# Kernel optimization log

Measured on AMD Instinct MI355X. Metric: run time of the kernel, lower is better.

The kernel has to match this reference:

```python
import jax, jax.numpy as jnp
import numpy as np

N, E, D, L, G, T = 50000, 600000, 128, 4, 512, 10
EPS = 1e-5


def setup_inputs() -> dict:
    key = jax.random.key(0)
    ks = jax.random.split(key, 20)
    s = lambda k, shp, fan: jax.random.normal(k, shp, jnp.float32) * (1.0 / np.sqrt(fan))
    inp = {
        'x': jax.random.normal(ks[0], (N, 3), jnp.float32),
        'edge_index': jax.random.randint(ks[1], (2, E), 0, N, jnp.int32),
        'batch': jnp.sort(jax.random.randint(ks[2], (N,), 0, G, jnp.int32)),
        'emb_W': s(ks[3], (3, D), 3),
        'emb_b': jnp.zeros((D,), jnp.float32),
        'conv_W': s(ks[4], (L, 12 * D, D), 12 * D),
        'conv_b': jnp.zeros((L, D), jnp.float32),
        'bn_gamma': jnp.ones((L, D), jnp.float32),
        'bn_beta': jnp.zeros((L, D), jnp.float32),
        'W1': s(ks[5], (D, D // 2), D), 'b1': jnp.zeros((D // 2,), jnp.float32),
        'W2': s(ks[6], (D // 2, D // 4), D // 2), 'b2': jnp.zeros((D // 4,), jnp.float32),
        'W3': s(ks[7], (D // 4, T), D // 4), 'b3': jnp.zeros((T,), jnp.float32),
    }
    return inp


def reference(x, edge_index, batch, emb_W, emb_b, conv_W, conv_b, bn_gamma, bn_beta,
              W1, b1, W2, b2, W3, b3):
    n = x.shape[0]
    src, dst = edge_index[0], edge_index[1]  # messages flow src(j) -> dst(i)
    deg = jax.ops.segment_sum(jnp.ones((src.shape[0],), x.dtype), dst, num_segments=n)
    delta = jnp.mean(jnp.log1p(deg))          # avg log-degree (PNA's avg_deg['log'])
    d = jnp.maximum(deg, 1.0)[:, None]        # clamp(min=1)
    log_d = jnp.log1p(d)
    amp, att = log_d / delta, delta / log_d   # amplification / attenuation scalers
    has_edge = (deg > 0)[:, None]

    h = x @ emb_W + emb_b                     # node_emb Linear(3, D)
    for l in range(conv_W.shape[0]):
        msg = h[src]                          # [E, D] gather
        s1 = jax.ops.segment_sum(msg, dst, num_segments=n)
        s2 = jax.ops.segment_sum(msg * msg, dst, num_segments=n)
        mean = s1 / d
        std = jnp.sqrt(jax.nn.relu(s2 / d - mean * mean) + EPS)
        mn = jnp.where(has_edge, jax.ops.segment_min(msg, dst, num_segments=n), 0.0)
        mx = jnp.where(has_edge, jax.ops.segment_max(msg, dst, num_segments=n), 0.0)
        aggs = jnp.concatenate([mean, mn, mx, std], axis=-1)                 # [N, 4D]
        out = jnp.concatenate([aggs, aggs * amp, aggs * att], axis=-1)       # [N, 12D]
        out = out @ conv_W[l] + conv_b[l]      # post_nn Linear(12D, D)
        mu = out.mean(axis=0)
        var = out.var(axis=0)
        out = (out - mu) * jax.lax.rsqrt(var + EPS) * bn_gamma[l] + bn_beta[l]
        h = jax.nn.relu(out) + h               # residual (dropout off: eval)

    # global_mean_pool over graphs
    gsum = jax.ops.segment_sum(h, batch, num_segments=G)
    cnt = jnp.maximum(jax.ops.segment_sum(jnp.ones((n,), h.dtype), batch, num_segments=G), 1.0)
    g = gsum / cnt[:, None]
    g = jax.nn.relu(g @ W1 + b1)
    g = jax.nn.relu(g @ W2 + b2)
    return g @ W3 + b3                         # source='image': no clamp
```

## Files before the change

### kernel.cpp

```cpp
#include <hip/hip_runtime.h>
#include <math.h>

#define NN 50000
#define NE 600000
#define DD 128
#define NL 4
#define NG 512
#define NT 10
#define EPSF 1e-5f

typedef __bf16 bf16x8 __attribute__((ext_vector_type(8)));
typedef float f32x4 __attribute__((ext_vector_type(4)));

__device__ __forceinline__ unsigned short f2bf(float x) {
    union { float f; unsigned u; } v; v.f = x;
    unsigned r = v.u + 0x7FFFu + ((v.u >> 16) & 1u);
    return (unsigned short)(r >> 16);
}
__device__ __forceinline__ unsigned pack_bf2(float a, float b) {
    return (unsigned)f2bf(a) | ((unsigned)f2bf(b) << 16);
}
__device__ __forceinline__ float bf_lo(unsigned v) {
    union { unsigned u; float f; } w; w.u = (v & 0xFFFFu) << 16; return w.f;
}
__device__ __forceinline__ float bf_hi(unsigned v) {
    union { unsigned u; float f; } w; w.u = v & 0xFFFF0000u; return w.f;
}
__device__ __forceinline__ void ld16(const void* g, void* l) {
    __builtin_amdgcn_global_load_lds(
        (const __attribute__((address_space(1))) unsigned int*)g,
        (__attribute__((address_space(3))) unsigned int*)l, 16, 0, 0);
}

__global__ void k_count(const int* __restrict__ dst, int* __restrict__ deg,
                        float* __restrict__ dsum, int E) {
    int e = blockIdx.x * blockDim.x + threadIdx.x;
    if (e == 0) *dsum = 0.f;
    if (e < E) atomicAdd(&deg[dst[e]], 1);
}

__global__ void k_scan_part(const int* __restrict__ deg, int* __restrict__ part, int n) {
    __shared__ int sm[256];
    int b = blockIdx.x, t = threadIdx.x;
    int base = b * 1024 + t * 4;
    int s = 0;
    #pragma unroll
    for (int j = 0; j < 4; j++) if (base + j < n) s += deg[base + j];
    sm[t] = s;
    __syncthreads();
    for (int off = 128; off > 0; off >>= 1) {
        if (t < off) sm[t] += sm[t + off];
        __syncthreads();
    }
    if (t == 0) part[b] = sm[0];
}

__global__ void k_scan_top(const int* __restrict__ part, int* __restrict__ offs,
                           int* __restrict__ row_ptr, int nb, int n) {
    if (threadIdx.x == 0) {
        int acc = 0;
        for (int i = 0; i < nb; i++) { offs[i] = acc; acc += part[i]; }
        row_ptr[n] = acc;
    }
}

__global__ void k_scan_apply(const int* __restrict__ deg, const int* __restrict__ offs,
                             int* __restrict__ row_ptr, int* __restrict__ cursor, int n) {
    __shared__ int sm[256];
    int b = blockIdx.x, t = threadIdx.x;
    int base = b * 1024 + t * 4;
    int v[4]; int s = 0;
    #pragma unroll
    for (int j = 0; j < 4; j++) { v[j] = (base + j < n) ? deg[base + j] : 0; s += v[j]; }
    sm[t] = s;
    __syncthreads();
    for (int off = 1; off < 256; off <<= 1) {
        int y = (t >= off) ? sm[t - off] : 0;
        __syncthreads();
        sm[t] += y;
        __syncthreads();
    }
    int run = offs[b] + sm[t] - s;
    #pragma unroll
    for (int j = 0; j < 4; j++) {
        if (base + j < n) { row_ptr[base + j] = run; cursor[base + j] = run; run += v[j]; }
    }
}

__global__ void k_fill(const int* __restrict__ src, const int* __restrict__ dst,
                       int* __restrict__ cursor, int* __restrict__ csr_src, int E) {
    int e = blockIdx.x * blockDim.x + threadIdx.x;
    if (e < E) {
        int d = dst[e];
        int pos = atomicAdd(&cursor[d], 1);
        csr_src[pos] = src[e];
    }
}

__global__ void k_delta(const int* __restrict__ deg, float* __restrict__ dsum, int n) {
    int i = blockIdx.x * blockDim.x + threadIdx.x;
    float v = (i < n) ? log1pf((float)deg[i]) : 0.f;
    #pragma unroll
    for (int off = 32; off > 0; off >>= 1) v += __shfl_down(v, off);
    if ((threadIdx.x & 63) == 0) atomicAdd(dsum, v);
}

__global__ void k_scalars(const int* __restrict__ deg, const float* __restrict__ dsum,
                          float* __restrict__ inv_d, float* __restrict__ amp,
                          float* __restrict__ att, int n) {
    int i = blockIdx.x * blockDim.x + threadIdx.x;
    if (i >= n) return;
    float delta = *dsum / (float)n;
    float d = fmaxf((float)deg[i], 1.f);
    float ld = log1pf(d);
    inv_d[i] = 1.f / d;
    amp[i] = ld / delta;
    att[i] = delta / ld;
}

__global__ void k_emb(const float* __restrict__ x, const float* __restrict__ W,
                      const float* __restrict__ b, float* __restrict__ h,
                      unsigned* __restrict__ hb2, int total2) {
    int i = blockIdx.x * blockDim.x + threadIdx.x;
    if (i >= total2) return;
    int node = i >> 6, c = (i & 63) * 2;
    float x0 = x[node * 3 + 0], x1 = x[node * 3 + 1], x2 = x[node * 3 + 2];
    float v0 = x0 * W[c] + x1 * W[DD + c] + x2 * W[2 * DD + c] + b[c];
    float v1 = x0 * W[c + 1] + x1 * W[DD + c + 1] + x2 * W[2 * DD + c + 1] + b[c + 1];
    ((float2*)h)[i] = make_float2(v0, v1);
    hb2[i] = pack_bf2(v0, v1);
}

__global__ void k_wconv(const float* __restrict__ W, unsigned short* __restrict__ Bt, int total) {
    int o = blockIdx.x * blockDim.x + threadIdx.x;
    if (o >= total) return;
    int l = o / 196608;
    int r = o % 196608;
    int j = r >> 16;
    int r2 = r & 65535;
    int n = r2 >> 9;
    int k = r2 & 511;
    Bt[o] = f2bf(W[(size_t)l * 196608 + (size_t)(j * 512 + k) * 128 + n]);
}

__global__ void k_agg(const unsigned* __restrict__ hb2, const int* __restrict__ row_ptr,
                      const int* __restrict__ csr_src, const float* __restrict__ inv_d,
                      unsigned* __restrict__ aggs_u, float* __restrict__ bn_zero) {
    int tid = threadIdx.x;
    if (blockIdx.x == 0) bn_zero[tid] = 0.f;
    int node = blockIdx.x * 4 + (tid >> 6);
    int t = tid & 63;
    int beg = row_ptr[node], end = row_ptr[node + 1];
    float s1a = 0.f, s1b = 0.f, s2a = 0.f, s2b = 0.f;
    float mna = INFINITY, mnb = INFINITY, mxa = -INFINITY, mxb = -INFINITY;
    int e = beg;
    for (; e + 1 < end; e += 2) {
        int sa = csr_src[e], sb = csr_src[e + 1];
        unsigned va = hb2[(size_t)sa * 64 + t];
        unsigned vb = hb2[(size_t)sb * 64 + t];
        float a0 = bf_lo(va), b0 = bf_hi(va);
        float a1 = bf_lo(vb), b1 = bf_hi(vb);
        s1a += a0 + a1; s2a += a0 * a0 + a1 * a1;
        mna = fminf(mna, fminf(a0, a1)); mxa = fmaxf(mxa, fmaxf(a0, a1));
        s1b += b0 + b1; s2b += b0 * b0 + b1 * b1;
        mnb = fminf(mnb, fminf(b0, b1)); mxb = fmaxf(mxb, fmaxf(b0, b1));
    }
    if (e < end) {
        int sa = csr_src[e];
        unsigned va = hb2[(size_t)sa * 64 + t];
        float a0 = bf_lo(va), b0 = bf_hi(va);
        s1a += a0; s2a += a0 * a0; mna = fminf(mna, a0); mxa = fmaxf(mxa, a0);
        s1b += b0; s2b += b0 * b0; mnb = fminf(mnb, b0); mxb = fmaxf(mxb, b0);
    }
    float id = inv_d[node];
    float meana = s1a * id, meanb = s1b * id;
    float sda = sqrtf(fmaxf(s2a * id - meana * meana, 0.f) + EPSF);
    float sdb = sqrtf(fmaxf(s2b * id - meanb * meanb, 0.f) + EPSF);
    if (beg == end) { mna = 0.f; mxa = 0.f; mnb = 0.f; mxb = 0.f; }
    unsigned* outr = aggs_u + (size_t)node * 256;
    outr[t]       = pack_bf2(meana, meanb);
    outr[64 + t]  = pack_bf2(mna, mnb);
    outr[128 + t] = pack_bf2(mxa, mxb);
    outr[192 + t] = pack_bf2(sda, sdb);
}

__global__ __launch_bounds__(256, 3) void k_gemm_mfma(
    const unsigned short* __restrict__ A, const unsigned short* __restrict__ Bt,
    const float* __restrict__ bias, const float* __restrict__ amp,
    const float* __restrict__ att, float* __restrict__ outp,
    float* __restrict__ bn_sum, float* __restrict__ bn_sq, int n) {
    __shared__ unsigned short As[128 * 32];
    __shared__ unsigned short Bs[3 * 64 * 32];
    int tid = threadIdx.x;
    int w = tid >> 6, lane = tid & 63;
    int wrow = w >> 1, wcol = w & 1;
    int quad = lane >> 4, l16 = lane & 15;
    int row0 = blockIdx.x * 128;
    int c0 = blockIdx.y * 64;

    f32x4 acc[4][2][3];
    #pragma unroll
    for (int rt = 0; rt < 4; rt++)
        #pragma unroll
        for (int ct = 0; ct < 2; ct++)
            #pragma unroll
            for (int j = 0; j < 3; j++) acc[rt][ct][j] = (f32x4)(0.f);

    const unsigned short* gA[2];
    int aLds[2];
    #pragma unroll
    for (int i = 0; i < 2; i++) {
        int c = i * 256 + tid;
        int row = c >> 2, kc = c & 3;
        gA[i] = A + (size_t)(row0 + row) * 512 + kc * 8;
        aLds[i] = c * 8;
    }
    const unsigned short* gB[3];
    int bLds[3];
    int bn_ = tid >> 2, bk = tid & 3;
    #pragma unroll
    for (int i = 0; i < 3; i++) {
        gB[i] = Bt + (size_t)(i * 128 + c0 + bn_) * 512 + bk * 8;
        bLds[i] = (i * 64 + bn_) * 32 + bk * 8;
    }
    int a_off[4];
    #pragma unroll
    for (int rt = 0; rt < 4; rt++)
        a_off[rt] = (wrow * 64 + rt * 16 + l16) * 32 + quad * 8;
    int b_off[2][3];
    #pragma unroll
    for (int ct = 0; ct < 2; ct++)
        #pragma unroll
        for (int j = 0; j < 3; j++)
            b_off[ct][j] = (j * 64 + wcol * 32 + ct * 16 + l16) * 32 + quad * 8;

    for (int k0 = 0; k0 < 512; k0 += 32) {
        __syncthreads();
        ld16(gA[0] + k0, &As[aLds[0]]);
        ld16(gA[1] + k0, &As[aLds[1]]);
        #pragma unroll
        for (int i = 0; i < 3; i++) ld16(gB[i] + k0, &Bs[bLds[i]]);
        __syncthreads();
        bf16x8 af[4];
        #pragma unroll
        for (int rt = 0; rt < 4; rt++) af[rt] = *(const bf16x8*)&As[a_off[rt]];
        #pragma unroll
        for (int ct = 0; ct < 2; ct++) {
            #pragma unroll
            for (int j = 0; j < 3; j++) {
                bf16x8 bf = *(const bf16x8*)&Bs[b_off[ct][j]];
                #pragma unroll
                for (int rt = 0; rt < 4; rt++)
                    acc[rt][ct][j] = __builtin_amdgcn_mfma_f32_16x16x32_bf16(
                        af[rt], bf, acc[rt][ct][j], 0, 0, 0);
            }
        }
    }

    float psum[2] = {0.f, 0.f}, psq[2] = {0.f, 0.f};
    #pragma unroll
    for (int rt = 0; rt < 4; rt++) {
        #pragma unroll
        for (int reg = 0; reg < 4; reg++) {
            int row = row0 + wrow * 64 + rt * 16 + quad * 4 + reg;
            if (row < n) {
                float am = amp[row], at = att[row];
                #pragma unroll
                for (int ct = 0; ct < 2; ct++) {
                    int col = c0 + wcol * 32 + ct * 16 + l16;
                    float v = acc[rt][ct][0][reg] + am * acc[rt][ct][1][reg]
                            + at * acc[rt][ct][2][reg] + bias[col];
                    outp[(size_t)row * DD + col] = v;
                    psum[ct] += v;
                    psq[ct] += v * v;
                }
            }
        }
    }
    #pragma unroll
    for (int ct = 0; ct < 2; ct++) {
        psum[ct] += __shfl_xor(psum[ct], 16, 64);
        psum[ct] += __shfl_xor(psum[ct], 32, 64);
        psq[ct]  += __shfl_xor(psq[ct], 16, 64);
        psq[ct]  += __shfl_xor(psq[ct], 32, 64);
    }
    if (quad == 0) {
        #pragma unroll
        for (int ct = 0; ct < 2; ct++) {
            int col = c0 + wcol * 32 + ct * 16 + l16;
            atomicAdd(&bn_sum[col], psum[ct]);
            atomicAdd(&bn_sq[col], psq[ct]);
        }
    }
}

__global__ void k_bnapply(const float* __restrict__ outp, const float* __restrict__ bn_sum,
                          const float* __restrict__ bn_sq, const float* __restrict__ gamma,
                          const float* __restrict__ beta, float* __restrict__ h,
                          unsigned* __restrict__ hb2, int total4) {
    int i = blockIdx.x * blockDim.x + threadIdx.x;
    if (i >= total4) return;
    int c = (i & 31) * 4;
    const float invn = 1.f / (float)NN;
    float4 o = ((const float4*)outp)[i];
    float4 hh = ((float4*)h)[i];
    float oo[4] = {o.x, o.y, o.z, o.w};
    float hs[4] = {hh.x, hh.y, hh.z, hh.w};
    #pragma unroll
    for (int j = 0; j < 4; j++) {
        float mu = bn_sum[c + j] * invn;
        float var = bn_sq[c + j] * invn - mu * mu;
        float sc = rsqrtf(var + EPSF) * gamma[c + j];
        float sh = beta[c + j] - mu * sc;
        hs[j] += fmaxf(oo[j] * sc + sh, 0.f);
    }
    ((float4*)h)[i] = make_float4(hs[0], hs[1], hs[2], hs[3]);
    hb2[i * 2]     = pack_bf2(hs[0], hs[1]);
    hb2[i * 2 + 1] = pack_bf2(hs[2], hs[3]);
}

__global__ void k_pool_mlp(const float* __restrict__ h, const int* __restrict__ batch,
                           const float* __restrict__ W1, const float* __restrict__ b1,
                           const float* __restrict__ W2, const float* __restrict__ b2,
                           const float* __restrict__ W3, const float* __restrict__ b3,
                           float* __restrict__ out, int n) {
    __shared__ float gvec[128];
    __shared__ float h1[64];
    __shared__ float h2[32];
    __shared__ int srange[2];
    int g = blockIdx.x;
    int t = threadIdx.x;
    if (t < 2) {
        int target = g + t;
        int lo = 0, hi = n;
        while (lo < hi) {
            int mid = (lo + hi) >> 1;
            if (batch[mid] < target) lo = mid + 1; else hi = mid;
        }
        srange[t] = lo;
    }
    __syncthreads();
    int s = srange[0], e = srange[1];
    float acc = 0.f;
    for (int i = s; i < e; i++) acc += h[(size_t)i * DD + t];
    float cnt = fmaxf((float)(e - s), 1.f);
    gvec[t] = acc / cnt;
    __syncthreads();
    if (t < 64) {
        float a = b1[t];
        for (int k = 0; k < 128; k++) a += gvec[k] * W1[k * 64 + t];
        h1[t] = fmaxf(a, 0.f);
    }
    __syncthreads();
    if (t < 32) {
        float a = b2[t];
        for (int k = 0; k < 64; k++) a += h1[k] * W2[k * 32 + t];
        h2[t] = fmaxf(a, 0.f);
    }
    __syncthreads();
    if (t < 10) {
        float a = b3[t];
        for (int k = 0; k < 32; k++) a += h2[k] * W3[k * 10 + t];
        out[g * NT + t] = a;
    }
}

extern "C" void kernel_launch(void* const* d_in, const int* in_sizes, int n_in,
                              void* d_out, int out_size, void* d_ws, size_t ws_size,
                              hipStream_t stream) {
    const float* x      = (const float*)d_in[0];
    const int*   eidx   = (const int*)d_in[1];
    const int*   batch  = (const int*)d_in[2];
    const float* emb_W  = (const float*)d_in[3];
    const float* emb_b  = (const float*)d_in[4];
    const float* conv_W = (const float*)d_in[5];
    const float* conv_b = (const float*)d_in[6];
    const float* bn_g   = (const float*)d_in[7];
    const float* bn_b   = (const float*)d_in[8];
    const float* W1 = (const float*)d_in[9];
    const float* b1 = (const float*)d_in[10];
    const float* W2 = (const float*)d_in[11];
    const float* b2 = (const float*)d_in[12];
    const float* W3 = (const float*)d_in[13];
    const float* b3 = (const float*)d_in[14];
    float* out = (float*)d_out;

    const int* src = eidx;
    const int* dst = eidx + NE;

    char* p = (char*)d_ws;
    auto carve = [&](size_t bytes) {
        void* r = (void*)p;
        p += (bytes + 255) & ~(size_t)255;
        return r;
    };
    int* deg      = (int*)carve(NN * 4);
    int* row_ptr  = (int*)carve((NN + 1) * 4);
    int* cursor   = (int*)carve(NN * 4);
    int* csr_src  = (int*)carve(NE * 4);
    int* part     = (int*)carve(64 * 4);
    int* offs     = (int*)carve(64 * 4);
    float* inv_d  = (float*)carve(NN * 4);
    float* amp    = (float*)carve(NN * 4);
    float* att    = (float*)carve(NN * 4);
    float* dsum   = (float*)carve(4);
    float* bn_sum = (float*)carve(DD * 4);
    float* bn_sq  = (float*)carve(DD * 4);
    float* h      = (float*)carve((size_t)NN * DD * 4);
    unsigned* hb2 = (unsigned*)carve((size_t)NN * 64 * 4);
    unsigned* aggs_u = (unsigned*)carve((size_t)NN * 256 * 4);
    float* outp   = (float*)carve((size_t)NN * DD * 4);
    unsigned short* Bt = (unsigned short*)carve((size_t)NL * 3 * 128 * 512 * 2);

    hipMemsetAsync(deg, 0, NN * 4, stream);

    const int NSB = (NN + 1023) / 1024;
    k_count<<<(NE + 255) / 256, 256, 0, stream>>>(dst, deg, dsum, NE);
    k_scan_part<<<NSB, 256, 0, stream>>>(deg, part, NN);
    k_scan_top<<<1, 64, 0, stream>>>(part, offs, row_ptr, NSB, NN);
    k_scan_apply<<<NSB, 256, 0, stream>>>(deg, offs, row_ptr, cursor, NN);
    k_fill<<<(NE + 255) / 256, 256, 0, stream>>>(src, dst, cursor, csr_src, NE);
    k_delta<<<(NN + 255) / 256, 256, 0, stream>>>(deg, dsum, NN);
    k_scalars<<<(NN + 255) / 256, 256, 0, stream>>>(deg, dsum, inv_d, amp, att, NN);
    k_emb<<<(NN * 64 + 255) / 256, 256, 0, stream>>>(x, emb_W, emb_b, h, hb2, NN * 64);
    k_wconv<<<(NL * 196608 + 255) / 256, 256, 0, stream>>>(conv_W, Bt, NL * 196608);

    dim3 gemm_grid((NN + 127) / 128, 2);
    for (int l = 0; l < NL; l++) {
        k_agg<<<(NN + 3) / 4, 256, 0, stream>>>(hb2, row_ptr, csr_src, inv_d, aggs_u, bn_sum);
        k_gemm_mfma<<<gemm_grid, 256, 0, stream>>>(
            (const unsigned short*)aggs_u, Bt + (size_t)l * 3 * 128 * 512,
            conv_b + l * DD, amp, att, outp, bn_sum, bn_sq, NN);
        k_bnapply<<<(NN * 32 + 255) / 256, 256, 0, stream>>>(
            outp, bn_sum, bn_sq, bn_g + l * DD, bn_b + l * DD, h, hb2, NN * 32);
    }

    k_pool_mlp<<<NG, 128, 0, stream>>>(h, batch, W1, b1, W2, b2, W3, b3, out, NN);
}
```

Measured before the change: 687.5 us.

## Load GEMM MFMA fragments directly from global memory, dropping LDS staging

The post-aggregation GEMM no longer stages A and B tiles through shared memory with global_load_lds and two barriers per K step. Each lane now loads its MFMA fragments straight from global memory into registers, and the launch-bounds occupancy hint is dropped. This removes barrier and LDS traffic but gives up data sharing across waves. Each A/B fragment is now fetched by two waves, and loads are 16-byte per row with 1 KB row strides, so coalescing and L2 pressure may worsen.

```diff
diff --git a/kernel.cpp b/kernel.cpp
--- a/kernel.cpp
+++ b/kernel.cpp
@@ -25,11 +25,6 @@
 }
 __device__ __forceinline__ float bf_hi(unsigned v) {
     union { unsigned u; float f; } w; w.u = v & 0xFFFF0000u; return w.f;
-}
-__device__ __forceinline__ void ld16(const void* g, void* l) {
-    __builtin_amdgcn_global_load_lds(
-        (const __attribute__((address_space(1))) unsigned int*)g,
-        (__attribute__((address_space(3))) unsigned int*)l, 16, 0, 0);
 }
 
 __global__ void k_count(const int* __restrict__ dst, int* __restrict__ deg,
@@ -184,13 +179,11 @@
     outr[192 + t] = pack_bf2(sda, sdb);
 }
 
-__global__ __launch_bounds__(256, 3) void k_gemm_mfma(
+__global__ __launch_bounds__(256) void k_gemm_mfma(
     const unsigned short* __restrict__ A, const unsigned short* __restrict__ Bt,
     const float* __restrict__ bias, const float* __restrict__ amp,
     const float* __restrict__ att, float* __restrict__ outp,
     float* __restrict__ bn_sum, float* __restrict__ bn_sq, int n) {
-    __shared__ unsigned short As[128 * 32];
-    __shared__ unsigned short Bs[3 * 64 * 32];
     int tid = threadIdx.x;
     int w = tid >> 6, lane = tid & 63;
     int wrow = w >> 1, wcol = w & 1;
@@ -206,55 +199,35 @@
             #pragma unroll
             for (int j = 0; j < 3; j++) acc[rt][ct][j] = (f32x4)(0.f);
 
-    const unsigned short* gA[2];
-    int aLds[2];
-    #pragma unroll
-    for (int i = 0; i < 2; i++) {
-        int c = i * 256 + tid;
-        int row = c >> 2, kc = c & 3;
-        gA[i] = A + (size_t)(row0 + row) * 512 + kc * 8;
-        aLds[i] = c * 8;
-    }
-    const unsigned short* gB[3];
-    int bLds[3];
-    int bn_ = tid >> 2, bk = tid & 3;
-    #pragma unroll
-    for (int i = 0; i < 3; i++) {
-        gB[i] = Bt + (size_t)(i * 128 + c0 + bn_) * 512 + bk * 8;
-        bLds[i] = (i * 64 + bn_) * 32 + bk * 8;
-    }
-    int a_off[4];
+    const unsigned short* pA[4];
     #pragma unroll
     for (int rt = 0; rt < 4; rt++)
-        a_off[rt] = (wrow * 64 + rt * 16 + l16) * 32 + quad * 8;
-    int b_off[2][3];
+        pA[rt] = A + (size_t)(row0 + wrow * 64 + rt * 16 + l16) * 512 + quad * 8;
+    const unsigned short* pB[2][3];
     #pragma unroll
     for (int ct = 0; ct < 2; ct++)
         #pragma unroll
         for (int j = 0; j < 3; j++)
-            b_off[ct][j] = (j * 64 + wcol * 32 + ct * 16 + l16) * 32 + quad * 8;
-
+            pB[ct][j] = Bt + (size_t)(j * 128 + c0 + wcol * 32 + ct * 16 + l16) * 512 + quad * 8;
+
+    #pragma unroll 1
     for (int k0 = 0; k0 < 512; k0 += 32) {
-        __syncthreads();
-        ld16(gA[0] + k0, &As[aLds[0]]);
-        ld16(gA[1] + k0, &As[aLds[1]]);
-        #pragma unroll
-        for (int i = 0; i < 3; i++) ld16(gB[i] + k0, &Bs[bLds[i]]);
-        __syncthreads();
         bf16x8 af[4];
         #pragma unroll
-        for (int rt = 0; rt < 4; rt++) af[rt] = *(const bf16x8*)&As[a_off[rt]];
-        #pragma unroll
-        for (int ct = 0; ct < 2; ct++) {
+        for (int rt = 0; rt < 4; rt++) af[rt] = *(const bf16x8*)(pA[rt] + k0);
+        bf16x8 bfr[2][3];
+        #pragma unroll
+        for (int ct = 0; ct < 2; ct++)
             #pragma unroll
-            for (int j = 0; j < 3; j++) {
-                bf16x8 bf = *(const bf16x8*)&Bs[b_off[ct][j]];
+            for (int j = 0; j < 3; j++) bfr[ct][j] = *(const bf16x8*)(pB[ct][j] + k0);
+        #pragma unroll
+        for (int ct = 0; ct < 2; ct++)
+            #pragma unroll
+            for (int j = 0; j < 3; j++)
                 #pragma unroll
                 for (int rt = 0; rt < 4; rt++)
                     acc[rt][ct][j] = __builtin_amdgcn_mfma_f32_16x16x32_bf16(
-                        af[rt], bf, acc[rt][ct][j], 0, 0, 0);
-            }
-        }
+                        af[rt], bfr[ct][j], acc[rt][ct][j], 0, 0, 0);
     }
 
     float psum[2] = {0.f, 0.f}, psq[2] = {0.f, 0.f};
```

Result: slower. 837.3 us (+21.8%).
